# Kernel tuning notes

Measured on AMD Instinct MI355X. Metric: run time of the kernel, lower is better.

## Reference

```python
import jax, jax.numpy as jnp
import numpy as np

HEAD, STACK = 8, 2
EPS = 1e-5


def _ln2d(x):
    # F.layer_norm(x, x.size()[1:]): normalize over (seq, feature) jointly, no affine
    m = jnp.mean(x, axis=(1, 2), keepdims=True)
    v = jnp.var(x, axis=(1, 2), keepdims=True)
    return (x - m) / jnp.sqrt(v + EPS)


def setup_inputs() -> dict:
    key = jax.random.key(0)
    ks = jax.random.split(key, 8)
    B, S, V, E, D, C = 64, 1024, 8000, 200, 200, 31
    g = lambda k, shape, sc: (jax.random.normal(k, shape, jnp.float32) * sc)
    return dict(
        x=jax.random.randint(ks[0], (B, S), 0, V),
        embed=g(ks[1], (V, E), 0.02),
        pos=g(ks[2], (S, E), 0.02),
        Wp=g(ks[3], (E, D), 0.05), bp=jnp.zeros((D,), jnp.float32),
        Wm=g(ks[4], (D * HEAD, D), 0.05), bm=jnp.zeros((D,), jnp.float32),
        W1=g(ks[5], (D, D), 0.05), b1=jnp.zeros((D,), jnp.float32),
        W2=g(ks[6], (D, D), 0.05), b2=jnp.zeros((D,), jnp.float32),
        Wd=g(ks[7], (D, C), 0.05), bd=jnp.zeros((C,), jnp.float32),
    )


def reference(x, embed, pos, Wp, bp, Wm, bm, W1, b1, W2, b2, Wd, bd):
    h = embed[x] + pos                       # [B,S,200]
    scale = jnp.sqrt(jnp.asarray(Wp.shape[1], jnp.float32))
    for _ in range(STACK):                   # weights shared across stacks (aliased in torch)
        r = h
        p = h @ Wp + bp                      # q = k = v (same aliased Linear in torch)
        a = jax.nn.softmax(jnp.einsum('bsd,btd->bst', p, p) / scale, axis=-1)
        c = jnp.einsum('bst,btd->bsd', a, p)  # [B,S,200]
        cat = jnp.tile(c, (1, 1, HEAD))       # all heads identical -> concat = tile
        h = _ln2d(cat @ Wm + bm + r)
        r = h
        ff = jax.nn.relu(h @ W1 + b1) @ W2 + b2
        h = _ln2d(ff + r)
    return h[:, -1, :] @ Wd + bd             # [B, class_num]; dropout = identity (eval)
```

## Files before the change

### kernel.cpp

```cpp
#include <hip/hip_runtime.h>
#include <cstddef>
#include <cstdint>
#include <cmath>

#define BDIM  64
#define SDIM  1024
#define DDIM  200
#define DPAD  224
#define PSTRIDE 232
#define CDIM  31
#define NSTACK 2
#define EPS   1e-5f
#define LN_N  204800.0f

typedef __attribute__((ext_vector_type(8))) short short8;
typedef __attribute__((ext_vector_type(4))) short short4_t;
typedef __attribute__((ext_vector_type(4))) float f32x4;

__device__ __forceinline__ short f2bf(float f) {
    union { float f; unsigned u; } v; v.f = f;
    unsigned r = v.u + 0x7FFFu + ((v.u >> 16) & 1u);
    return (short)(r >> 16);
}
__device__ __forceinline__ float bf2f(short s) {
    union { unsigned u; float f; } v; v.u = ((unsigned)(unsigned short)s) << 16;
    return v.f;
}
__device__ __forceinline__ unsigned cvtpk_bf16(float a, float b) {
    unsigned r;
    asm volatile("v_cvt_pk_bf16_f32 %0, %1, %2" : "=v"(r) : "v"(a), "v"(b));
    return r;
}
__device__ __forceinline__ void gload_lds16(const short* g, short* l) {
    __builtin_amdgcn_global_load_lds(
        (const __attribute__((address_space(1))) void*)g,
        (__attribute__((address_space(3))) void*)l, 16, 0, 0);
}

__global__ void prep_kernel(const float* __restrict__ Wp, const float* __restrict__ bp,
                            const float* __restrict__ Wm, const float* __restrict__ bm,
                            const float* __restrict__ W1, const float* __restrict__ b1,
                            const float* __restrict__ W2, const float* __restrict__ b2,
                            short* __restrict__ WtP, short* __restrict__ WtM,
                            short* __restrict__ Wt1, short* __restrict__ Wt2,
                            float* __restrict__ bpP, float* __restrict__ bmP,
                            float* __restrict__ b1P, float* __restrict__ b2P,
                            float* __restrict__ csP, float* __restrict__ cs1)
{
    int idx = blockIdx.x * 256 + threadIdx.x;
    if (idx >= DPAD * DPAD) return;
    int n = idx / DPAD, k = idx - n * DPAD;
    bool valid = (n < DDIM) && (k < DDIM);
    WtP[idx] = valid ? f2bf(Wp[(size_t)k * DDIM + n]) : 0;
    Wt1[idx] = valid ? f2bf(W1[(size_t)k * DDIM + n]) : 0;
    Wt2[idx] = valid ? f2bf(W2[(size_t)k * DDIM + n]) : 0;
    float s = 0.f;
    if (valid) {
        #pragma unroll
        for (int blk = 0; blk < 8; ++blk)
            s += Wm[(size_t)(blk * DDIM + k) * DDIM + n];
    }
    WtM[idx] = valid ? f2bf(s) : 0;
    if (idx < DPAD) {
        bpP[idx] = idx < DDIM ? bp[idx] : 0.f;
        bmP[idx] = idx < DDIM ? bm[idx] : 0.f;
        b1P[idx] = idx < DDIM ? b1[idx] : 0.f;
        b2P[idx] = idx < DDIM ? b2[idx] : 0.f;
        float sp = 0.f, s1 = 0.f;
        if (idx < DDIM) {
            for (int kk = 0; kk < DDIM; ++kk) {
                sp += bf2f(f2bf(Wp[(size_t)kk * DDIM + idx]));
                s1 += bf2f(f2bf(W1[(size_t)kk * DDIM + idx]));
            }
        }
        csP[idx] = sp;
        cs1[idx] = s1;
    }
}

__global__ void embed_kernel(const int* __restrict__ x, const float* __restrict__ embed,
                             const float* __restrict__ pos, short* __restrict__ h)
{
    const int total = BDIM * SDIM * (DPAD / 4);
    for (int i = blockIdx.x * 256 + threadIdx.x; i < total; i += gridDim.x * 256) {
        const int row = i / (DPAD / 4);
        const int n0  = (i - row * (DPAD / 4)) * 4;
        short4_t o;
        if (n0 >= DDIM) {
            o[0] = o[1] = o[2] = o[3] = 0;
        } else {
            const int s = row & (SDIM - 1);
            const int tok = x[row];
            const float4 e  = *(const float4*)(embed + (size_t)tok * DDIM + n0);
            const float4 p4 = *(const float4*)(pos + (size_t)s * DDIM + n0);
            o[0] = f2bf(e.x + p4.x); o[1] = f2bf(e.y + p4.y);
            o[2] = f2bf(e.z + p4.z); o[3] = f2bf(e.w + p4.w);
        }
        *(short4_t*)(h + (size_t)row * DPAD + n0) = o;
    }
}

#define WSLICE 7168
__global__ __launch_bounds__(256, 3)
void gemm_bf(const short* __restrict__ act, const float* __restrict__ actParts,
             const short* __restrict__ Wt, const float* __restrict__ bias,
             const float* __restrict__ csW,
             const short* __restrict__ res, const float* __restrict__ resParts,
             short* __restrict__ out, float* __restrict__ parts,
             int doRelu, int outStride)
{
    __shared__ short WB[2][WSLICE];

    const int tid  = threadIdx.x;
    const int wave = tid >> 6, lane = tid & 63;
    const int lo   = lane & 15, hi = lane >> 4;
    const int mblk = blockIdx.x * 128;
    const int m0   = mblk + wave * 32;

    auto stage = [&](int ks, int buf) {
        for (int c = wave; c < 14; c += 4) {
            int row = c * 16 + (lane >> 2);
            int kc  = (lane & 3) ^ ((row >> 1) & 3);
            gload_lds16(Wt + (size_t)row * DPAD + ks * 32 + kc * 8,
                        &WB[buf][c * 512 + lane * 8]);
        }
    };

    f32x4 acc[2][14];
    #pragma unroll
    for (int mt = 0; mt < 2; ++mt)
        #pragma unroll
        for (int nt = 0; nt < 14; ++nt) acc[mt][nt] = (f32x4){0.f, 0.f, 0.f, 0.f};

    stage(0, 0);
    __syncthreads();

    #pragma unroll
    for (int ks = 0; ks < 7; ++ks) {
        const int cur = ks & 1;
        if (ks < 6) stage(ks + 1, cur ^ 1);

        short8 af[2];
        #pragma unroll
        for (int mt = 0; mt < 2; ++mt)
            af[mt] = *(const short8*)(act + (size_t)(m0 + mt * 16 + lo) * DPAD
                                      + ks * 32 + hi * 8);
        #pragma unroll
        for (int nt = 0; nt < 14; ++nt) {
            int brow = nt * 16 + lo;
            short8 bf_ = *(const short8*)&WB[cur][brow * 32
                                                  + ((hi * 8) ^ (((brow >> 1) & 3) << 3))];
            acc[0][nt] = __builtin_amdgcn_mfma_f32_16x16x32_bf16(af[0], bf_, acc[0][nt], 0, 0, 0);
            acc[1][nt] = __builtin_amdgcn_mfma_f32_16x16x32_bf16(af[1], bf_, acc[1][nt], 0, 0, 0);
        }
        __syncthreads();
    }

    const int bb = mblk >> 10;
    float inv_a = 1.f, corr = 0.f;
    if (actParts) {
        float mean = actParts[bb * 2] / LN_N;
        inv_a = rsqrtf(actParts[bb * 2 + 1] / LN_N - mean * mean + EPS);
        corr = mean * inv_a;
    }
    float mean_r = 0.f, inv_r = 1.f;
    if (resParts) {
        mean_r = resParts[bb * 2] / LN_N;
        inv_r = rsqrtf(resParts[bb * 2 + 1] / LN_N - mean_r * mean_r + EPS);
    }

    float s = 0.f, s2 = 0.f;
    #pragma unroll
    for (int mt = 0; mt < 2; ++mt) {
        #pragma unroll
        for (int nt = 0; nt < 14; ++nt) {
            const int n = nt * 16 + lo;
            const float bn = bias[n];
            const float cw = actParts ? csW[n] : 0.f;
            float v[4];
            #pragma unroll
            for (int r = 0; r < 4; ++r)
                v[r] = acc[mt][nt][r] * inv_a + bn - corr * cw;
            if (res) {
                #pragma unroll
                for (int r = 0; r < 4; ++r) {
                    int m = m0 + mt * 16 + hi * 4 + r;
                    v[r] += (bf2f(res[(size_t)m * DPAD + n]) - mean_r) * inv_r;
                }
            }
            if (doRelu)
                #pragma unroll
                for (int r = 0; r < 4; ++r) v[r] = fmaxf(v[r], 0.f);
            if (n >= DDIM)
                #pragma unroll
                for (int r = 0; r < 4; ++r) v[r] = 0.f;
            if (parts)
                #pragma unroll
                for (int r = 0; r < 4; ++r) { s += v[r]; s2 = fmaf(v[r], v[r], s2); }
            #pragma unroll
            for (int r = 0; r < 4; ++r) {
                int m = m0 + mt * 16 + hi * 4 + r;
                out[(size_t)m * outStride + n] = f2bf(v[r]);
            }
        }
    }

    if (parts) {
        __shared__ float rs[4], rq[4];
        #pragma unroll
        for (int off = 32; off; off >>= 1) {
            s  += __shfl_down(s, off);
            s2 += __shfl_down(s2, off);
        }
        if (lane == 0) { rs[wave] = s; rq[wave] = s2; }
        __syncthreads();
        if (tid == 0) {
            atomicAdd(&parts[bb * 2],     rs[0] + rs[1] + rs[2] + rs[3]);
            atomicAdd(&parts[bb * 2 + 1], rq[0] + rq[1] + rq[2] + rq[3]);
        }
    }
}

__global__ void vt_kernel(const short* __restrict__ p, short* __restrict__ pt)
{
    __shared__ short T[32][33];
    const int b  = blockIdx.z;
    const int s0 = blockIdx.x * 32;
    const int d0 = blockIdx.y * 32;
    const int t  = threadIdx.x;
    const int row = t >> 3, c4 = (t & 7) * 4;
    short4_t v = *(const short4_t*)(p + ((size_t)b * SDIM + s0 + row) * PSTRIDE + d0 + c4);
    #pragma unroll
    for (int j = 0; j < 4; ++j) T[row][c4 + j] = v[j];
    __syncthreads();
    short4_t o;
    #pragma unroll
    for (int j = 0; j < 4; ++j) o[j] = T[c4 + j][row];
    *(short4_t*)(pt + ((size_t)b * DPAD + d0 + row) * SDIM + s0 + c4) = o;
}

__global__ __launch_bounds__(256, 2)
void attn_kernel(const short* __restrict__ pbf, const short* __restrict__ pt,
                 short* __restrict__ c, float qscale)
{
    __shared__ short Kbuf[2][7680];
    __shared__ short Vbuf[2][6656];

    const int bid = blockIdx.x;
    const int wg  = (bid & 7) * 64 + (bid >> 3);
    const int b   = wg >> 3;
    const int q0  = (wg & 7) * 128;

    const int tid  = threadIdx.x;
    const int wave = tid >> 6;
    const int lane = tid & 63;
    const int lo   = lane & 15;
    const int hi   = lane >> 4;

    const short* pb  = pbf + (size_t)b * SDIM * PSTRIDE;
    const short* ptb = pt  + (size_t)b * DPAD * SDIM;

    auto stage = [&](int kt2, int bufIdx) {
        const short* ks = pb + (size_t)kt2 * 32 * PSTRIDE + lane * 8;
        #pragma unroll
        for (int i = 0; i < 15; ++i)
            gload_lds16(ks + i * 512, &Kbuf[bufIdx][i * 512]);
        #pragma unroll
        for (int i = 0; i < 13; ++i) {
            int e = i * 512 + lane * 8;
            int d = e >> 5;
            int cc = (e & 31) ^ (((d >> 1) & 3) << 3);
            gload_lds16(ptb + (size_t)d * SDIM + kt2 * 32 + cc, &Vbuf[bufIdx][i * 512]);
        }
    };

    short8 qf[2][7];
    #pragma unroll
    for (int qt = 0; qt < 2; ++qt)
        #pragma unroll
        for (int ks = 0; ks < 7; ++ks) {
            short8 q = *(const short8*)(pb + (size_t)(q0 + wave * 32 + qt * 16 + lo) * PSTRIDE
                                        + ks * 32 + hi * 8);
            short8 qs;
            #pragma unroll
            for (int j = 0; j < 8; ++j) qs[j] = f2bf(bf2f(q[j]) * qscale);
            qf[qt][ks] = qs;
        }

    f32x4 o[2][13];
    float m[2], ell[2];
    #pragma unroll
    for (int qt = 0; qt < 2; ++qt) {
        #pragma unroll
        for (int n = 0; n < 13; ++n) o[qt][n] = (f32x4){0.f, 0.f, 0.f, 0.f};
        m[qt] = -1e30f; ell[qt] = 0.f;
    }

    if (wave == 0) stage(0, 0);
    __syncthreads();

    for (int kt = 0; kt < 32; ++kt) {
        const int cur = kt & 1;
        if (kt < 31 && wave == ((kt + 1) & 3)) stage(kt + 1, cur ^ 1);

        f32x4 sacc[2][2];
        #pragma unroll
        for (int qt = 0; qt < 2; ++qt)
            #pragma unroll
            for (int t = 0; t < 2; ++t) sacc[qt][t] = (f32x4){0.f, 0.f, 0.f, 0.f};
        __builtin_amdgcn_s_setprio(1);
        #pragma unroll
        for (int t = 0; t < 2; ++t)
            #pragma unroll
            for (int ks = 0; ks < 7; ++ks) {
                short8 kf = *(const short8*)(&Kbuf[cur][(t * 16 + lo) * PSTRIDE + ks * 32 + hi * 8]);
                sacc[0][t] = __builtin_amdgcn_mfma_f32_16x16x32_bf16(kf, qf[0][ks], sacc[0][t], 0, 0, 0);
                sacc[1][t] = __builtin_amdgcn_mfma_f32_16x16x32_bf16(kf, qf[1][ks], sacc[1][t], 0, 0, 0);
            }
        __builtin_amdgcn_s_setprio(0);

        short8 pa[2];
        #pragma unroll
        for (int qt = 0; qt < 2; ++qt) {
            float mx = fmaxf(fmaxf(fmaxf(sacc[qt][0][0], sacc[qt][0][1]),
                                   fmaxf(sacc[qt][0][2], sacc[qt][0][3])),
                             fmaxf(fmaxf(sacc[qt][1][0], sacc[qt][1][1]),
                                   fmaxf(sacc[qt][1][2], sacc[qt][1][3])));
            mx = fmaxf(mx, __shfl_xor(mx, 16));
            mx = fmaxf(mx, __shfl_xor(mx, 32));
            if (__any(mx > m[qt] + 11.5f)) {
                float mn = fmaxf(m[qt], mx);
                float al = exp2f(m[qt] - mn);
                m[qt] = mn; ell[qt] *= al;
                float alr[4];
                #pragma unroll
                for (int r = 0; r < 4; ++r) alr[r] = __shfl(al, hi * 4 + r);
                #pragma unroll
                for (int n = 0; n < 13; ++n)
                    #pragma unroll
                    for (int r = 0; r < 4; ++r) o[qt][n][r] *= alr[r];
            }
            float p[2][4]; float rsum = 0.f;
            #pragma unroll
            for (int t = 0; t < 2; ++t)
                #pragma unroll
                for (int r = 0; r < 4; ++r) {
                    p[t][r] = exp2f(sacc[qt][t][r] - m[qt]);
                    rsum += p[t][r];
                }
            rsum += __shfl_xor(rsum, 16);
            rsum += __shfl_xor(rsum, 32);
            ell[qt] += rsum;
            unsigned pk01_0 = cvtpk_bf16(p[0][0], p[0][1]);
            unsigned pk23_0 = cvtpk_bf16(p[0][2], p[0][3]);
            unsigned pk01_1 = cvtpk_bf16(p[1][0], p[1][1]);
            unsigned pk23_1 = cvtpk_bf16(p[1][2], p[1][3]);
            const int srcA = lo + ((hi & 1) * 2) * 16;
            const int srcB = srcA + 16;
            int a0 = __shfl((int)pk01_0, srcA), a1 = __shfl((int)pk01_1, srcA);
            int b0 = __shfl((int)pk23_0, srcA), b1 = __shfl((int)pk23_1, srcA);
            int c0 = __shfl((int)pk01_0, srcB), c1 = __shfl((int)pk01_1, srcB);
            int d0 = __shfl((int)pk23_0, srcB), d1 = __shfl((int)pk23_1, srcB);
            const bool thi = (hi >> 1) != 0;
            union { short8 s; int u[4]; } pu;
            pu.u[0] = thi ? a1 : a0;
            pu.u[1] = thi ? b1 : b0;
            pu.u[2] = thi ? c1 : c0;
            pu.u[3] = thi ? d1 : d0;
            pa[qt] = pu.s;
        }

        __builtin_amdgcn_s_setprio(1);
        #pragma unroll
        for (int n = 0; n < 13; ++n) {
            int d = n * 16 + lo;
            int addr = d * 32 + ((hi * 8) ^ (((d >> 1) & 3) << 3));
            short8 vf = *(const short8*)(&Vbuf[cur][addr]);
            o[0][n] = __builtin_amdgcn_mfma_f32_16x16x32_bf16(pa[0], vf, o[0][n], 0, 0, 0);
            o[1][n] = __builtin_amdgcn_mfma_f32_16x16x32_bf16(pa[1], vf, o[1][n], 0, 0, 0);
        }
        __builtin_amdgcn_s_setprio(0);

        __syncthreads();
    }

    #pragma unroll
    for (int qt = 0; qt < 2; ++qt) {
        float inv_l = 1.f / ell[qt];
        float invr[4];
        #pragma unroll
        for (int r = 0; r < 4; ++r) invr[r] = __shfl(inv_l, hi * 4 + r);
        #pragma unroll
        for (int n = 0; n < 13; ++n) {
            int dcol = n * 16 + lo;
            #pragma unroll
            for (int r = 0; r < 4; ++r) {
                size_t row = (size_t)b * SDIM + q0 + wave * 32 + qt * 16 + hi * 4 + r;
                c[row * DPAD + dcol] = f2bf(o[qt][n][r] * invr[r]);
            }
        }
        #pragma unroll
        for (int r = 0; r < 4; ++r) {
            size_t row = (size_t)b * SDIM + q0 + wave * 32 + qt * 16 + hi * 4 + r;
            c[row * DPAD + 208 + lo] = 0;
        }
    }
}

__global__ void final_kernel(const short* __restrict__ y, const float* __restrict__ parts,
                             const float* __restrict__ Wd, const float* __restrict__ bd,
                             float* __restrict__ out)
{
    const int b = blockIdx.x;
    const float sum = parts[b * 2], sq = parts[b * 2 + 1];
    const float mean = sum / LN_N;
    const float inv  = rsqrtf(sq / LN_N - mean * mean + EPS);
    __shared__ float hrow[DDIM];
    const short* row = y + ((size_t)b * SDIM + SDIM - 1) * DPAD;
    for (int d = threadIdx.x; d < DDIM; d += blockDim.x)
        hrow[d] = (bf2f(row[d]) - mean) * inv;
    __syncthreads();
    if (threadIdx.x < CDIM) {
        float acc = bd[threadIdx.x];
        for (int d = 0; d < DDIM; ++d)
            acc = fmaf(hrow[d], Wd[(size_t)d * CDIM + threadIdx.x], acc);
        out[(size_t)b * CDIM + threadIdx.x] = acc;
    }
}

extern "C" void kernel_launch(void* const* d_in, const int* in_sizes, int n_in,
                              void* d_out, int out_size, void* d_ws, size_t ws_size,
                              hipStream_t stream)
{
    const int*   x     = (const int*)  d_in[0];
    const float* embed = (const float*)d_in[1];
    const float* pos   = (const float*)d_in[2];
    const float* Wp    = (const float*)d_in[3];
    const float* bp    = (const float*)d_in[4];
    const float* Wm    = (const float*)d_in[5];
    const float* bm    = (const float*)d_in[6];
    const float* W1    = (const float*)d_in[7];
    const float* b1    = (const float*)d_in[8];
    const float* W2    = (const float*)d_in[9];
    const float* b2    = (const float*)d_in[10];
    const float* Wd    = (const float*)d_in[11];
    const float* bd    = (const float*)d_in[12];
    float* out = (float*)d_out;

    const size_t HB = (size_t)BDIM * SDIM * DPAD;
    const size_t PB = (size_t)BDIM * SDIM * PSTRIDE;

    short* h_bf  = (short*)d_ws;
    short* p_bf  = h_bf  + HB;
    short* pt    = p_bf  + PB;
    short* cb_bf = pt    + HB;
    short* yA    = cb_bf + HB;
    short* yB    = yA    + HB;
    short* WtP   = yB + HB;
    short* WtM   = WtP + DPAD * DPAD;
    short* Wt1   = WtM + DPAD * DPAD;
    short* Wt2   = Wt1 + DPAD * DPAD;
    float* bpP   = (float*)(Wt2 + DPAD * DPAD);
    float* bmP   = bpP + DPAD;
    float* b1P   = bmP + DPAD;
    float* b2P   = b1P + DPAD;
    float* csP   = b2P + DPAD;
    float* cs1   = csP + DPAD;
    float* parts = cs1 + DPAD;
    const size_t need = (size_t)((char*)(parts + 4 * BDIM * 2) - (char*)d_ws);
    if (ws_size < need) return;

    float* pA1 = parts;
    float* pB1 = parts + BDIM * 2;
    float* pA2 = parts + 2 * BDIM * 2;
    float* pB2 = parts + 3 * BDIM * 2;

    prep_kernel<<<dim3((DPAD * DPAD + 255) / 256), dim3(256), 0, stream>>>(
        Wp, bp, Wm, bm, W1, b1, W2, b2, WtP, WtM, Wt1, Wt2, bpP, bmP, b1P, b2P, csP, cs1);
    embed_kernel<<<dim3(2048), dim3(256), 0, stream>>>(x, embed, pos, h_bf);
    hipMemsetAsync(parts, 0, 4 * BDIM * 2 * sizeof(float), stream);

    const float qscale = 1.44269504f / sqrtf((float)DDIM);
    const dim3 tgrid(SDIM / 32, DPAD / 32, BDIM);

    gemm_bf<<<dim3(512), dim3(256), 0, stream>>>(h_bf, nullptr, WtP, bpP, nullptr,
                                                 nullptr, nullptr, p_bf, nullptr, 0, PSTRIDE);
    vt_kernel<<<tgrid, dim3(256), 0, stream>>>(p_bf, pt);
    attn_kernel<<<dim3(512), dim3(256), 0, stream>>>(p_bf, pt, cb_bf, qscale);
    gemm_bf<<<dim3(512), dim3(256), 0, stream>>>(cb_bf, nullptr, WtM, bmP, nullptr,
                                                 h_bf, nullptr, yA, pA1, 0, DPAD);
    gemm_bf<<<dim3(512), dim3(256), 0, stream>>>(yA, pA1, Wt1, b1P, cs1,
                                                 nullptr, nullptr, cb_bf, nullptr, 1, DPAD);
    gemm_bf<<<dim3(512), dim3(256), 0, stream>>>(cb_bf, nullptr, Wt2, b2P, nullptr,
                                                 yA, pA1, yB, pB1, 0, DPAD);
    gemm_bf<<<dim3(512), dim3(256), 0, stream>>>(yB, pB1, WtP, bpP, csP,
                                                 nullptr, nullptr, p_bf, nullptr, 0, PSTRIDE);
    vt_kernel<<<tgrid, dim3(256), 0, stream>>>(p_bf, pt);
    attn_kernel<<<dim3(512), dim3(256), 0, stream>>>(p_bf, pt, cb_bf, qscale);
    gemm_bf<<<dim3(512), dim3(256), 0, stream>>>(cb_bf, nullptr, WtM, bmP, nullptr,
                                                 yB, pB1, h_bf, pA2, 0, DPAD);
    gemm_bf<<<dim3(512), dim3(256), 0, stream>>>(h_bf, pA2, Wt1, b1P, cs1,
                                                 nullptr, nullptr, cb_bf, nullptr, 1, DPAD);
    gemm_bf<<<dim3(512), dim3(256), 0, stream>>>(cb_bf, nullptr, Wt2, b2P, nullptr,
                                                 h_bf, pA2, yA, pB2, 0, DPAD);
    final_kernel<<<dim3(BDIM), dim3(64), 0, stream>>>(yA, pB2, Wd, bd, out);
}
```

Baseline: 433.3 us.

## Retile GEMM waves to 2x2 layout and spread attention K/V staging across waves

The projection GEMM now splits its four waves into a 2x2 grid, each computing 64 rows by 112 columns instead of 32 rows by all 224 columns. Each B fragment read from LDS now feeds four MFMAs instead of two, which cuts LDS traffic per MFMA. The attention kernel now has all four waves stage K/V tiles cooperatively each iteration, instead of one rotating wave issuing all the loads. This balances load-issue work across waves but makes every wave pay some staging cost on every iteration.

```diff
diff --git a/kernel.cpp b/kernel.cpp
--- a/kernel.cpp
+++ b/kernel.cpp
@@ -114,8 +114,10 @@
     const int tid  = threadIdx.x;
     const int wave = tid >> 6, lane = tid & 63;
     const int lo   = lane & 15, hi = lane >> 4;
+    const int wm   = wave >> 1, wn = wave & 1;
     const int mblk = blockIdx.x * 128;
-    const int m0   = mblk + wave * 32;
+    const int mbase = mblk + wm * 64;
+    const int nbase = wn * 112;
 
     auto stage = [&](int ks, int buf) {
         for (int c = wave; c < 14; c += 4) {
@@ -126,11 +128,11 @@
         }
     };
 
-    f32x4 acc[2][14];
-    #pragma unroll
-    for (int mt = 0; mt < 2; ++mt)
-        #pragma unroll
-        for (int nt = 0; nt < 14; ++nt) acc[mt][nt] = (f32x4){0.f, 0.f, 0.f, 0.f};
+    f32x4 acc[4][7];
+    #pragma unroll
+    for (int mt = 0; mt < 4; ++mt)
+        #pragma unroll
+        for (int nt = 0; nt < 7; ++nt) acc[mt][nt] = (f32x4){0.f, 0.f, 0.f, 0.f};
 
     stage(0, 0);
     __syncthreads();
@@ -140,18 +142,19 @@
         const int cur = ks & 1;
         if (ks < 6) stage(ks + 1, cur ^ 1);
 
-        short8 af[2];
-        #pragma unroll
-        for (int mt = 0; mt < 2; ++mt)
-            af[mt] = *(const short8*)(act + (size_t)(m0 + mt * 16 + lo) * DPAD
+        short8 af[4];
+        #pragma unroll
+        for (int mt = 0; mt < 4; ++mt)
+            af[mt] = *(const short8*)(act + (size_t)(mbase + mt * 16 + lo) * DPAD
                                       + ks * 32 + hi * 8);
         #pragma unroll
-        for (int nt = 0; nt < 14; ++nt) {
-            int brow = nt * 16 + lo;
+        for (int nt = 0; nt < 7; ++nt) {
+            int brow = nbase + nt * 16 + lo;
             short8 bf_ = *(const short8*)&WB[cur][brow * 32
                                                   + ((hi * 8) ^ (((brow >> 1) & 3) << 3))];
-            acc[0][nt] = __builtin_amdgcn_mfma_f32_16x16x32_bf16(af[0], bf_, acc[0][nt], 0, 0, 0);
-            acc[1][nt] = __builtin_amdgcn_mfma_f32_16x16x32_bf16(af[1], bf_, acc[1][nt], 0, 0, 0);
+            #pragma unroll
+            for (int mt = 0; mt < 4; ++mt)
+                acc[mt][nt] = __builtin_amdgcn_mfma_f32_16x16x32_bf16(af[mt], bf_, acc[mt][nt], 0, 0, 0);
         }
         __syncthreads();
     }
@@ -171,10 +174,10 @@
 
     float s = 0.f, s2 = 0.f;
     #pragma unroll
-    for (int mt = 0; mt < 2; ++mt) {
-        #pragma unroll
-        for (int nt = 0; nt < 14; ++nt) {
-            const int n = nt * 16 + lo;
+    for (int mt = 0; mt < 4; ++mt) {
+        #pragma unroll
+        for (int nt = 0; nt < 7; ++nt) {
+            const int n = nbase + nt * 16 + lo;
             const float bn = bias[n];
             const float cw = actParts ? csW[n] : 0.f;
             float v[4];
@@ -184,7 +187,7 @@
             if (res) {
                 #pragma unroll
                 for (int r = 0; r < 4; ++r) {
-                    int m = m0 + mt * 16 + hi * 4 + r;
+                    int m = mbase + mt * 16 + hi * 4 + r;
                     v[r] += (bf2f(res[(size_t)m * DPAD + n]) - mean_r) * inv_r;
                 }
             }
@@ -199,7 +202,7 @@
                 for (int r = 0; r < 4; ++r) { s += v[r]; s2 = fmaf(v[r], v[r], s2); }
             #pragma unroll
             for (int r = 0; r < 4; ++r) {
-                int m = m0 + mt * 16 + hi * 4 + r;
+                int m = mbase + mt * 16 + hi * 4 + r;
                 out[(size_t)m * outStride + n] = f2bf(v[r]);
             }
         }
@@ -261,12 +264,12 @@
     const short* ptb = pt  + (size_t)b * DPAD * SDIM;
 
     auto stage = [&](int kt2, int bufIdx) {
-        const short* ks = pb + (size_t)kt2 * 32 * PSTRIDE + lane * 8;
-        #pragma unroll
-        for (int i = 0; i < 15; ++i)
-            gload_lds16(ks + i * 512, &Kbuf[bufIdx][i * 512]);
-        #pragma unroll
-        for (int i = 0; i < 13; ++i) {
+        const short* ksrc = pb + (size_t)kt2 * 32 * PSTRIDE + lane * 8;
+        #pragma unroll
+        for (int i = wave; i < 15; i += 4)
+            gload_lds16(ksrc + i * 512, &Kbuf[bufIdx][i * 512]);
+        #pragma unroll
+        for (int i = wave; i < 13; i += 4) {
             int e = i * 512 + lane * 8;
             int d = e >> 5;
             int cc = (e & 31) ^ (((d >> 1) & 3) << 3);
@@ -296,12 +299,12 @@
         m[qt] = -1e30f; ell[qt] = 0.f;
     }
 
-    if (wave == 0) stage(0, 0);
+    stage(0, 0);
     __syncthreads();
 
     for (int kt = 0; kt < 32; ++kt) {
         const int cur = kt & 1;
-        if (kt < 31 && wave == ((kt + 1) & 3)) stage(kt + 1, cur ^ 1);
+        if (kt < 31) stage(kt + 1, cur ^ 1);
 
         f32x4 sacc[2][2];
         #pragma unroll
```

Result: slower. 510.4 us (+17.8%).

## Fuse FFN GEMMs into one kernel keeping ReLU intermediate in LDS

Applied to the files above, without the earlier changes.

Adds an ffn_bf kernel that computes relu(LN(h)@W1+b1) into shared memory and immediately multiplies by W2 with the residual and LayerNorm partial sums, replacing two gemm_bf launches per stack. This removes the global write and re-read of the intermediate activation and one launch per stack. It also prefetches the next A-fragment from global one k-step ahead in gemm_bf. The fused kernel uses 64-row tiles with a large LDS footprint, which can lower occupancy and means weights are reloaded across twice as many blocks.

```diff
diff --git a/kernel.cpp b/kernel.cpp
--- a/kernel.cpp
+++ b/kernel.cpp
@@ -132,19 +132,23 @@
         #pragma unroll
         for (int nt = 0; nt < 14; ++nt) acc[mt][nt] = (f32x4){0.f, 0.f, 0.f, 0.f};
 
+    short8 af[2], afn[2];
+    #pragma unroll
+    for (int mt = 0; mt < 2; ++mt)
+        af[mt] = *(const short8*)(act + (size_t)(m0 + mt * 16 + lo) * DPAD + hi * 8);
     stage(0, 0);
     __syncthreads();
 
     #pragma unroll
     for (int ks = 0; ks < 7; ++ks) {
         const int cur = ks & 1;
-        if (ks < 6) stage(ks + 1, cur ^ 1);
-
-        short8 af[2];
-        #pragma unroll
-        for (int mt = 0; mt < 2; ++mt)
-            af[mt] = *(const short8*)(act + (size_t)(m0 + mt * 16 + lo) * DPAD
-                                      + ks * 32 + hi * 8);
+        if (ks < 6) {
+            #pragma unroll
+            for (int mt = 0; mt < 2; ++mt)
+                afn[mt] = *(const short8*)(act + (size_t)(m0 + mt * 16 + lo) * DPAD
+                                           + (ks + 1) * 32 + hi * 8);
+            stage(ks + 1, cur ^ 1);
+        }
         #pragma unroll
         for (int nt = 0; nt < 14; ++nt) {
             int brow = nt * 16 + lo;
@@ -154,6 +158,7 @@
             acc[1][nt] = __builtin_amdgcn_mfma_f32_16x16x32_bf16(af[1], bf_, acc[1][nt], 0, 0, 0);
         }
         __syncthreads();
+        if (ks < 6) { af[0] = afn[0]; af[1] = afn[1]; }
     }
 
     const int bb = mblk >> 10;
@@ -206,6 +211,136 @@
     }
 
     if (parts) {
+        __shared__ float rs[4], rq[4];
+        #pragma unroll
+        for (int off = 32; off; off >>= 1) {
+            s  += __shfl_down(s, off);
+            s2 += __shfl_down(s2, off);
+        }
+        if (lane == 0) { rs[wave] = s; rq[wave] = s2; }
+        __syncthreads();
+        if (tid == 0) {
+            atomicAdd(&parts[bb * 2],     rs[0] + rs[1] + rs[2] + rs[3]);
+            atomicAdd(&parts[bb * 2 + 1], rq[0] + rq[1] + rq[2] + rq[3]);
+        }
+    }
+}
+
+#define Y1S 232
+__global__ __launch_bounds__(256, 2)
+void ffn_bf(const short* __restrict__ act, const float* __restrict__ actParts,
+            const float* __restrict__ csW1,
+            const short* __restrict__ Wt1, const float* __restrict__ b1,
+            const short* __restrict__ Wt2, const float* __restrict__ b2,
+            short* __restrict__ out, float* __restrict__ parts)
+{
+    __shared__ short WB[2][WSLICE];
+    __shared__ short Y1[64 * Y1S];
+
+    const int tid  = threadIdx.x;
+    const int wave = tid >> 6, lane = tid & 63;
+    const int lo   = lane & 15, hi = lane >> 4;
+    const int mblk = blockIdx.x * 64;
+    const int m0   = mblk + wave * 16;
+    const int bb   = mblk >> 10;
+
+    auto stageW = [&](const short* W, int ks, int buf) {
+        for (int c = wave; c < 14; c += 4) {
+            int row = c * 16 + (lane >> 2);
+            int kc  = (lane & 3) ^ ((row >> 1) & 3);
+            gload_lds16(W + (size_t)row * DPAD + ks * 32 + kc * 8,
+                        &WB[buf][c * 512 + lane * 8]);
+        }
+    };
+
+    const float mean_a = actParts[bb * 2] / LN_N;
+    const float inv_a  = rsqrtf(actParts[bb * 2 + 1] / LN_N - mean_a * mean_a + EPS);
+    const float corr   = mean_a * inv_a;
+
+    f32x4 acc[14];
+    #pragma unroll
+    for (int nt = 0; nt < 14; ++nt) acc[nt] = (f32x4){0.f, 0.f, 0.f, 0.f};
+
+    short8 af = *(const short8*)(act + (size_t)(m0 + lo) * DPAD + hi * 8);
+    short8 afn;
+    stageW(Wt1, 0, 0);
+    __syncthreads();
+
+    #pragma unroll
+    for (int ks = 0; ks < 7; ++ks) {
+        const int cur = ks & 1;
+        if (ks < 6) {
+            afn = *(const short8*)(act + (size_t)(m0 + lo) * DPAD + (ks + 1) * 32 + hi * 8);
+            stageW(Wt1, ks + 1, cur ^ 1);
+        } else {
+            stageW(Wt2, 0, cur ^ 1);
+        }
+        #pragma unroll
+        for (int nt = 0; nt < 14; ++nt) {
+            int brow = nt * 16 + lo;
+            short8 bf_ = *(const short8*)&WB[cur][brow * 32
+                                                  + ((hi * 8) ^ (((brow >> 1) & 3) << 3))];
+            acc[nt] = __builtin_amdgcn_mfma_f32_16x16x32_bf16(af, bf_, acc[nt], 0, 0, 0);
+        }
+        __syncthreads();
+        if (ks < 6) af = afn;
+    }
+
+    #pragma unroll
+    for (int nt = 0; nt < 14; ++nt) {
+        const int n = nt * 16 + lo;
+        const float bn = b1[n];
+        const float cw = csW1[n];
+        #pragma unroll
+        for (int r = 0; r < 4; ++r) {
+            float v = fmaxf(acc[nt][r] * inv_a + bn - corr * cw, 0.f);
+            Y1[(wave * 16 + hi * 4 + r) * Y1S + n] = f2bf(v);
+        }
+    }
+    __syncthreads();
+
+    #pragma unroll
+    for (int nt = 0; nt < 14; ++nt) acc[nt] = (f32x4){0.f, 0.f, 0.f, 0.f};
+
+    #pragma unroll
+    for (int ks = 0; ks < 7; ++ks) {
+        const int cur = (ks + 1) & 1;
+        if (ks < 6) stageW(Wt2, ks + 1, cur ^ 1);
+        short8 a2 = *(const short8*)&Y1[(wave * 16 + lo) * Y1S + ks * 32 + hi * 8];
+        #pragma unroll
+        for (int nt = 0; nt < 14; ++nt) {
+            int brow = nt * 16 + lo;
+            short8 bf_ = *(const short8*)&WB[cur][brow * 32
+                                                  + ((hi * 8) ^ (((brow >> 1) & 3) << 3))];
+            acc[nt] = __builtin_amdgcn_mfma_f32_16x16x32_bf16(a2, bf_, acc[nt], 0, 0, 0);
+        }
+        __syncthreads();
+    }
+
+    float s = 0.f, s2 = 0.f;
+    #pragma unroll
+    for (int nt = 0; nt < 14; ++nt) {
+        const int n = nt * 16 + lo;
+        const float bn = b2[n];
+        float v[4];
+        #pragma unroll
+        for (int r = 0; r < 4; ++r) {
+            int m = m0 + hi * 4 + r;
+            v[r] = acc[nt][r] + bn + (bf2f(act[(size_t)m * DPAD + n]) - mean_a) * inv_a;
+        }
+        if (n >= DDIM)
+            #pragma unroll
+            for (int r = 0; r < 4; ++r) v[r] = 0.f;
+        #pragma unroll
+        for (int r = 0; r < 4; ++r) { s += v[r]; s2 = fmaf(v[r], v[r], s2); }
+        #pragma unroll
+        for (int r = 0; r < 4; ++r) {
+            int m = m0 + hi * 4 + r;
+            out[(size_t)m * DPAD + n] = f2bf(v[r]);
+        }
+    }
+
+    {
         __shared__ float rs[4], rq[4];
         #pragma unroll
         for (int off = 32; off; off >>= 1) {
@@ -489,19 +624,13 @@
     attn_kernel<<<dim3(512), dim3(256), 0, stream>>>(p_bf, pt, cb_bf, qscale);
     gemm_bf<<<dim3(512), dim3(256), 0, stream>>>(cb_bf, nullptr, WtM, bmP, nullptr,
                                                  h_bf, nullptr, yA, pA1, 0, DPAD);
-    gemm_bf<<<dim3(512), dim3(256), 0, stream>>>(yA, pA1, Wt1, b1P, cs1,
-                                                 nullptr, nullptr, cb_bf, nullptr, 1, DPAD);
-    gemm_bf<<<dim3(512), dim3(256), 0, stream>>>(cb_bf, nullptr, Wt2, b2P, nullptr,
-                                                 yA, pA1, yB, pB1, 0, DPAD);
+    ffn_bf<<<dim3(1024), dim3(256), 0, stream>>>(yA, pA1, cs1, Wt1, b1P, Wt2, b2P, yB, pB1);
     gemm_bf<<<dim3(512), dim3(256), 0, stream>>>(yB, pB1, WtP, bpP, csP,
                                                  nullptr, nullptr, p_bf, nullptr, 0, PSTRIDE);
     vt_kernel<<<tgrid, dim3(256), 0, stream>>>(p_bf, pt);
     attn_kernel<<<dim3(512), dim3(256), 0, stream>>>(p_bf, pt, cb_bf, qscale);
     gemm_bf<<<dim3(512), dim3(256), 0, stream>>>(cb_bf, nullptr, WtM, bmP, nullptr,
                                                  yB, pB1, h_bf, pA2, 0, DPAD);
-    gemm_bf<<<dim3(512), dim3(256), 0, stream>>>(h_bf, pA2, Wt1, b1P, cs1,
-                                                 nullptr, nullptr, cb_bf, nullptr, 1, DPAD);
-    gemm_bf<<<dim3(512), dim3(256), 0, stream>>>(cb_bf, nullptr, Wt2, b2P, nullptr,
-                                                 h_bf, pA2, yA, pB2, 0, DPAD);
+    ffn_bf<<<dim3(1024), dim3(256), 0, stream>>>(h_bf, pA2, cs1, Wt1, b1P, Wt2, b2P, yA, pB2);
     final_kernel<<<dim3(BDIM), dim3(64), 0, stream>>>(yA, pB2, Wd, bd, out);
 }
```

Result: faster. 398.0 us (-8.1%).
